# Kernel optimization log

Measured on AMD Instinct MI355X. Metric: run time of the kernel, lower is better.

The kernel has to match this reference:

```python
import math
import jax, jax.numpy as jnp
import numpy as np

DIM = 256; DEPTH = 5; FANOUT = 10; VOCAB = 257
B = 16; T = 2048
NEXP = 8; HID = 512; TOPK = 2; TEMP = 1.0; HEADS = 2
CAPACITY = math.ceil(B * TOPK / NEXP * 1.1)  # capacity-based dispatch, =5
LAYER_SIZES = [FANOUT ** l for l in range(DEPTH)]  # [1,10,100,1000,10000]


def setup_inputs() -> dict:
    key = jax.random.key(0)
    ks = iter(jax.random.split(key, 64))
    def p(shape, scale=0.02):
        return jax.random.normal(next(ks), shape, jnp.float32) * scale
    inp = {
        'tokens': jax.random.randint(next(ks), (B, T), 0, VOCAB),
        'embed': p((VOCAB, DIM)),
        'pin_w': p((DIM, DIM)), 'pin_b': jnp.zeros(DIM, jnp.float32),
        'pch_w': p((DIM, DIM)), 'pch_b': jnp.zeros(DIM, jnp.float32),
        'depth_bias': p((DEPTH, DIM)),
        'q_w': p((DIM, DIM)), 'q_b': jnp.zeros(DIM, jnp.float32),
        'k_w': p((DIM, DIM)), 'k_b': jnp.zeros(DIM, jnp.float32),
        'v_w': p((DIM, DIM)), 'v_b': jnp.zeros(DIM, jnp.float32),
        'o_w': p((DIM, DIM)), 'o_b': jnp.zeros(DIM, jnp.float32),
        'level_gate': jnp.zeros(DEPTH, jnp.float32),
        'depth_gate': jnp.zeros((DEPTH, DIM), jnp.float32),
        'in_proj_w': p((DIM, 3 * DIM)), 'in_proj_b': jnp.zeros(3 * DIM, jnp.float32),
        'out_proj_w': p((DIM, DIM)), 'out_proj_b': jnp.zeros(DIM, jnp.float32),
        'ln_g': jnp.ones(DIM, jnp.float32), 'ln_b': jnp.zeros(DIM, jnp.float32),
        'ic_gate': jnp.zeros(1, jnp.float32),
        'gate_w': p((DIM, NEXP)), 'gate_b': jnp.zeros(NEXP, jnp.float32),
        'ew1': p((NEXP, DIM, HID)), 'eb1': jnp.zeros((NEXP, HID), jnp.float32),
        'ew2': p((NEXP, HID, DIM)), 'eb2': jnp.zeros((NEXP, DIM), jnp.float32),
        'hw1': p((DIM, DIM)), 'hb1': jnp.zeros(DIM, jnp.float32),
        'hw2': p((DIM, VOCAB)), 'hb2': jnp.zeros(VOCAB, jnp.float32),
    }
    return inp


def _fractal(context, pin_w, pin_b, pch_w, pch_b, depth_bias, q_w, q_b, k_w, k_b,
             v_w, v_b, o_w, o_b, level_gate, depth_gate,
             in_proj_w, in_proj_b, out_proj_w, out_proj_b, ln_g, ln_b, ic_gate):
    Bc = context.shape[0]
    base = context @ pin_w + pin_b                       # [B,D]
    y_next = None
    level_means = [None] * DEPTH
    inv_sqrt_d = 1.0 / math.sqrt(DIM)
    for l in reversed(range(DEPTH)):
        n = LAYER_SIZES[l]
        if l == DEPTH - 1:
            child_agg = jnp.zeros((Bc, n, DIM), context.dtype)
        else:
            yg = y_next.reshape(Bc, n, FANOUT, DIM)      # children grouped per parent
            q = (base + depth_bias[l]) @ q_w + q_b       # [B,D], shared across nodes
            k = yg @ k_w + k_b
            v = yg @ v_w + v_b
            att = jax.nn.softmax(jnp.einsum('bd,bnfd->bnf', q, k) * inv_sqrt_d, axis=-1)
            child_agg = jax.nn.sigmoid(depth_gate[l]) * jnp.einsum('bnf,bnfd->bnd', att, v)
        gate = jax.nn.sigmoid(level_gate[l])
        upd = (base[:, None, :] + depth_bias[l][None, None, :] + child_agg @ pch_w + pch_b) * gate
        y = jax.nn.relu(upd) @ o_w + o_b                 # [B,n,D]
        level_means[l] = y.mean(axis=1)
        y_next = y
    root = y_next[:, 0, :]                               # n==1 at level 0
    # interconnect: MHA over per-level means [B,DEPTH,D]
    z = jnp.stack(level_means, axis=1)
    qkv = z @ in_proj_w + in_proj_b
    qh, kh, vh = jnp.split(qkv, 3, axis=-1)
    hd = DIM // HEADS
    def to_heads(t):
        return t.reshape(Bc, DEPTH, HEADS, hd).transpose(0, 2, 1, 3)
    qh, kh, vh = to_heads(qh), to_heads(kh), to_heads(vh)
    aw = jax.nn.softmax(jnp.einsum('bhqd,bhkd->bhqk', qh, kh) / math.sqrt(hd), axis=-1)
    z2 = jnp.einsum('bhqk,bhkd->bhqd', aw, vh).transpose(0, 2, 1, 3).reshape(Bc, DEPTH, DIM)
    z2 = z2 @ out_proj_w + out_proj_b
    zs = z + z2
    mu = zs.mean(-1, keepdims=True)
    var = ((zs - mu) ** 2).mean(-1, keepdims=True)
    zn = (zs - mu) / jnp.sqrt(var + 1e-5) * ln_g + ln_b
    return root + jax.nn.sigmoid(ic_gate) * zn[:, 0, :]


def _moe(ctx, gate_w, gate_b, ew1, eb1, ew2, eb2):
    scaled = (ctx @ gate_w + gate_b) / TEMP
    top_vals, top_idx = jax.lax.top_k(scaled, TOPK)      # [B,K]
    gs = jax.nn.softmax(top_vals, axis=-1)               # [B,K], strictly > 0
    out = jnp.zeros_like(ctx)
    for e in range(NEXP):                                # fixed small expert loop
        sflat = jnp.where(top_idx == e, gs, -1.0).reshape(-1)   # [B*K]
        vals, pos = jax.lax.top_k(sflat, CAPACITY)       # capacity-limited dispatch
        w = jnp.where(vals > 0.0, vals, 0.0)             # drop unassigned/overflow
        tok = pos // TOPK
        xin = ctx[tok]                                   # [cap,D]
        eo = jax.nn.relu(xin @ ew1[e] + eb1[e]) @ ew2[e] + eb2[e]
        out = out.at[tok].add(eo * w[:, None])
    return out


def reference(tokens, embed, pin_w, pin_b, pch_w, pch_b, depth_bias,
              q_w, q_b, k_w, k_b, v_w, v_b, o_w, o_b, level_gate, depth_gate,
              in_proj_w, in_proj_b, out_proj_w, out_proj_b, ln_g, ln_b, ic_gate,
              gate_w, gate_b, ew1, eb1, ew2, eb2, hw1, hb1, hw2, hb2):
    x = embed[tokens]                                    # [B,T,D]
    context = x.mean(axis=1)                             # [B,D]
    root = _fractal(context, pin_w, pin_b, pch_w, pch_b, depth_bias, q_w, q_b,
                    k_w, k_b, v_w, v_b, o_w, o_b, level_gate, depth_gate,
                    in_proj_w, in_proj_b, out_proj_w, out_proj_b, ln_g, ln_b, ic_gate)
    root = root + _moe(root, gate_w, gate_b, ew1, eb1, ew2, eb2)
    h = x + root[:, None, :]                             # per-token logits from context + token emb
    logits = jax.nn.relu(h @ hw1 + hb1) @ hw2 + hb2      # [B,T,V]
    return logits
```

## Files before the change

### kernel.cpp

```cpp
#include <hip/hip_runtime.h>
#include <hip/hip_bf16.h>
#include <math.h>

#define DIM    256
#define DEPTH  5
#define FANOUT 10
#define VOCAB  257
#define BB     16
#define TT     2048
#define NEXP   8
#define HID    512
#define TOPK   2
#define CAP    5

__device__ __forceinline__ float sigm(float x) { return 1.f / (1.f + expf(-x)); }

__device__ __forceinline__ void mv8x2(const float* sv, const float* __restrict__ W,
                                      int kseg, int cq, float red[16][DIM]) {
  const float* Wp = W + (size_t)kseg * 16 * DIM + cq * 4;
  float4 acc = {0.f, 0.f, 0.f, 0.f};
#pragma unroll 1
  for (int h = 0; h < 2; ++h) {
    float4 wv[8];
#pragma unroll
    for (int i = 0; i < 8; ++i)
      wv[i] = *(const float4*)(Wp + (size_t)(h * 8 + i) * DIM);
#pragma unroll
    for (int i = 0; i < 8; ++i) {
      float s = sv[kseg * 16 + h * 8 + i];
      acc.x = fmaf(s, wv[i].x, acc.x);
      acc.y = fmaf(s, wv[i].y, acc.y);
      acc.z = fmaf(s, wv[i].z, acc.z);
      acc.w = fmaf(s, wv[i].w, acc.w);
    }
    __builtin_amdgcn_sched_barrier(0);
  }
  *(float4*)&red[kseg][cq * 4] = acc;
}

__device__ __forceinline__ float sum16(const float red[16][DIM], int d) {
  float s = 0.f;
#pragma unroll
  for (int g = 0; g < 16; ++g) s += red[g][d];
  return s;
}

__global__ void __launch_bounds__(1024) k_fractal(
    const int* __restrict__ tokens, const float* __restrict__ embed,
    const float* __restrict__ pin_w, const float* __restrict__ pin_b,
    const float* __restrict__ pch_w, const float* __restrict__ pch_b,
    const float* __restrict__ depth_bias,
    const float* __restrict__ v_w, const float* __restrict__ v_b,
    const float* __restrict__ o_w, const float* __restrict__ o_b,
    const float* __restrict__ level_gate, const float* __restrict__ depth_gate,
    const float* __restrict__ in_proj_w, const float* __restrict__ in_proj_b,
    const float* __restrict__ out_proj_w, const float* __restrict__ out_proj_b,
    const float* __restrict__ ln_g, const float* __restrict__ ln_b,
    const float* __restrict__ ic_gate,
    float* __restrict__ rootA, float* __restrict__ root2,
    int* __restrict__ bidx, int* __restrict__ boff) {
  int bx = blockIdx.x;
  int tid = threadIdx.x;
  int xcd = bx & 7, slot = bx >> 3;
  __shared__ int cnt[VOCAB];
  __shared__ float sv[DIM];
  __shared__ float basev[DIM];
  __shared__ float ym[DEPTH][DIM];
  __shared__ float q0v[DIM], kh[DEPTH][DIM], vh[DEPTH][DIM];
  __shared__ float red11[4][11][DIM];
  __shared__ float zsv[DIM];
  __shared__ float aw[16];
  __shared__ float redl[8];
  __shared__ int offb[VOCAB + 1];
  __shared__ int woff[VOCAB];
  float (*red16)[DIM] = reinterpret_cast<float(*)[DIM]>(&red11[0][0][0]);

  if (xcd == 1) {
    if (slot < BB) {
      int b = slot;
      for (int i = tid; i < VOCAB; i += 1024) cnt[i] = 0;
      __syncthreads();
      for (int t = tid; t < TT; t += 1024) atomicAdd(&cnt[tokens[b * TT + t]], 1);
      __syncthreads();
      if (tid == 0) {
        int a = 0;
        for (int v = 0; v < VOCAB; ++v) { offb[v] = a; a += cnt[v]; }
        offb[VOCAB] = a;
      }
      __syncthreads();
      if (tid <= VOCAB) boff[b * (VOCAB + 1) + tid] = offb[tid];
      if (tid < VOCAB) woff[tid] = offb[tid];
      __syncthreads();
      for (int t = tid; t < TT; t += 1024) {
        int tok = tokens[b * TT + t];
        int p = atomicAdd(&woff[tok], 1);
        bidx[b * TT + p] = t;
      }
    }
    return;
  }
  if (xcd != 0) return;
  if (slot >= BB) {
    int w = slot - BB;
    float sx = 0.f, sy = 0.f, sz = 0.f, sw = 0.f;
#pragma unroll 1
    for (int q = 0; q < 3; ++q) {
      int r = w * 3 + q;
      if (r >= 37) break;
      const float* W; int n = 16384;
      if (r < 4)       W = pin_w      + (size_t)r * 16384;
      else if (r < 8)  W = pch_w      + (size_t)(r - 4) * 16384;
      else if (r < 12) W = v_w        + (size_t)(r - 8) * 16384;
      else if (r < 16) W = o_w        + (size_t)(r - 12) * 16384;
      else if (r < 20) W = out_proj_w + (size_t)(r - 16) * 16384;
      else if (r < 32) W = in_proj_w  + (size_t)(r - 20) * 16384;
      else { W = embed + (size_t)(r - 32) * 16384; n = 65792 - (r - 32) * 16384;
             if (n > 16384) n = 16384; }
      const float4* src = (const float4*)W + tid;
#pragma unroll
      for (int k = 0; k < 4; ++k) {
        int p = tid * 4 + k * 4096;
        if (p + 4 <= n) {
          float4 v = src[k * 1024];
          sx += v.x; sy += v.y; sz += v.z; sw += v.w;
        }
      }
    }
    asm volatile("" :: "v"(sx), "v"(sy), "v"(sz), "v"(sw));
    return;
  }

  int b = slot;
  int d = tid & 255;
  int ks = tid >> 8;
  int k0 = ks * 64;
  int kseg = tid >> 6;
  int cq = tid & 63;

  for (int i = tid; i < VOCAB; i += 1024) cnt[i] = 0;
  __syncthreads();
  for (int t = tid; t < TT; t += 1024) atomicAdd(&cnt[tokens[b * TT + t]], 1);
  __syncthreads();
  {
    const float* Ep = embed + (size_t)kseg * 16 * DIM + cq * 4;
    float4 acc = {0.f, 0.f, 0.f, 0.f};
#pragma unroll 1
    for (int h = 0; h < 2; ++h) {
      float4 ev[8];
#pragma unroll
      for (int i = 0; i < 8; ++i)
        ev[i] = *(const float4*)(Ep + (size_t)(h * 8 + i) * DIM);
#pragma unroll
      for (int i = 0; i < 8; ++i) {
        float cv = (float)cnt[kseg * 16 + h * 8 + i];
        acc.x = fmaf(cv, ev[i].x, acc.x);
        acc.y = fmaf(cv, ev[i].y, acc.y);
        acc.z = fmaf(cv, ev[i].z, acc.z);
        acc.w = fmaf(cv, ev[i].w, acc.w);
      }
      __builtin_amdgcn_sched_barrier(0);
    }
    *(float4*)&red16[kseg][cq * 4] = acc;
  }
  __syncthreads();
  if (ks == 0) {
    float s = sum16(red16, d);
    s = fmaf((float)cnt[256], embed[(size_t)256 * DIM + d], s);
    sv[d] = s * (1.0f / (float)TT);
  }
  __syncthreads();

  mv8x2(sv, pin_w, kseg, cq, red16);
  __syncthreads();
  if (ks == 0) {
    float base = sum16(red16, d) + pin_b[d];
    basev[d] = base;
    float u = (base + depth_bias[4 * DIM + d] + pch_b[d]) * sigm(level_gate[4]);
    sv[d] = fmaxf(u, 0.f);
  }
  __syncthreads();
  mv8x2(sv, o_w, kseg, cq, red16);
  __syncthreads();
  if (ks == 0) {
    float y = sum16(red16, d) + o_b[d];
    ym[4][d] = y;
    sv[d] = y;
  }
  __syncthreads();
  for (int l = 3; l >= 0; --l) {
    mv8x2(sv, v_w, kseg, cq, red16);
    __syncthreads();
    if (ks == 0) {
      float vv = sum16(red16, d) + v_b[d];
      sv[d] = sigm(depth_gate[l * DIM + d]) * vv;
    }
    __syncthreads();
    mv8x2(sv, pch_w, kseg, cq, red16);
    __syncthreads();
    if (ks == 0) {
      float t = sum16(red16, d) + pch_b[d];
      float u = (basev[d] + depth_bias[l * DIM + d] + t) * sigm(level_gate[l]);
      sv[d] = fmaxf(u, 0.f);
    }
    __syncthreads();
    mv8x2(sv, o_w, kseg, cq, red16);
    __syncthreads();
    if (ks == 0) {
      float y = sum16(red16, d) + o_b[d];
      ym[l][d] = y;
      sv[d] = y;
    }
    __syncthreads();
  }
  {
    float aq = 0.f;
    float ak0 = 0.f, ak1 = 0.f, ak2 = 0.f, ak3 = 0.f, ak4 = 0.f;
    float av0 = 0.f, av1 = 0.f, av2 = 0.f, av3 = 0.f, av4 = 0.f;
#pragma unroll
    for (int h = 0; h < 8; ++h) {
      int kb = k0 + h * 8;
      float wq[8], wk[8], wv8[8];
#pragma unroll
      for (int i = 0; i < 8; ++i) {
        const float* wrow = in_proj_w + (size_t)(kb + i) * 768;
        wq[i] = wrow[d]; wk[i] = wrow[256 + d]; wv8[i] = wrow[512 + d];
      }
#pragma unroll
      for (int i = 0; i < 8; ++i) {
        float z0 = ym[0][kb + i];
        aq  = fmaf(z0, wq[i], aq);
        ak0 = fmaf(z0, wk[i], ak0);
        av0 = fmaf(z0, wv8[i], av0);
        float z1 = ym[1][kb + i];
        ak1 = fmaf(z1, wk[i], ak1);
        av1 = fmaf(z1, wv8[i], av1);
        float z2 = ym[2][kb + i];
        ak2 = fmaf(z2, wk[i], ak2);
        av2 = fmaf(z2, wv8[i], av2);
        float z3 = ym[3][kb + i];
        ak3 = fmaf(z3, wk[i], ak3);
        av3 = fmaf(z3, wv8[i], av3);
        float z4 = ym[4][kb + i];
        ak4 = fmaf(z4, wk[i], ak4);
        av4 = fmaf(z4, wv8[i], av4);
      }
    }
    red11[ks][0][d] = ak0; red11[ks][1][d] = ak1; red11[ks][2][d] = ak2;
    red11[ks][3][d] = ak3; red11[ks][4][d] = ak4;
    red11[ks][5][d] = av0; red11[ks][6][d] = av1; red11[ks][7][d] = av2;
    red11[ks][8][d] = av3; red11[ks][9][d] = av4;
    red11[ks][10][d] = aq;
  }
  __syncthreads();
  for (int idx = tid; idx < 11 * DIM; idx += 1024) {
    int c = idx >> 8, dd = idx & 255;
    float sum = red11[0][c][dd] + red11[1][c][dd] + red11[2][c][dd] + red11[3][c][dd];
    if (c < 5)       kh[c][dd]     = sum + in_proj_b[256 + dd];
    else if (c < 10) vh[c - 5][dd] = sum + in_proj_b[512 + dd];
    else             q0v[dd]       = sum + in_proj_b[dd];
  }
  __syncthreads();
  {
    int wid = tid >> 6;
    if (wid < 10) {
      int h = wid / 5, l = wid - h * 5;
      int lane = tid & 63;
      float s = q0v[h * 128 + lane] * kh[l][h * 128 + lane];
      s = fmaf(q0v[h * 128 + 64 + lane], kh[l][h * 128 + 64 + lane], s);
      for (int o = 32; o > 0; o >>= 1) s += __shfl_down(s, o, 64);
      if (lane == 0) aw[wid] = s * 0.08838834764831845f;
    }
  }
  __syncthreads();
  if (tid < 2) {
    float m = aw[tid * 5];
    for (int l = 1; l < 5; ++l) m = fmaxf(m, aw[tid * 5 + l]);
    float e[5], ssum = 0.f;
    for (int l = 0; l < 5; ++l) { e[l] = expf(aw[tid * 5 + l] - m); ssum += e[l]; }
    for (int l = 0; l < 5; ++l) aw[tid * 5 + l] = e[l] / ssum;
  }
  __syncthreads();
  if (ks == 0) {
    int h = d >> 7;
    float z2 = 0.f;
    for (int l = 0; l < 5; ++l) z2 = fmaf(aw[h * 5 + l], vh[l][d], z2);
    sv[d] = z2;
  }
  __syncthreads();
  mv8x2(sv, out_proj_w, kseg, cq, red16);
  __syncthreads();
  if (ks == 0) {
    float z2p = sum16(red16, d) + out_proj_b[d];
    zsv[d] = ym[0][d] + z2p;
  }
  __syncthreads();
  float zs = 0.f, df = 0.f, mu = 0.f;
  if (tid < 256) {
    zs = zsv[tid];
    float v = zs;
    for (int o = 32; o > 0; o >>= 1) v += __shfl_down(v, o, 64);
    if ((tid & 63) == 0) redl[tid >> 6] = v;
  }
  __syncthreads();
  if (tid < 256) {
    mu = (redl[0] + redl[1] + redl[2] + redl[3]) * (1.f / 256.f);
    df = zs - mu;
  }
  __syncthreads();
  if (tid < 256) {
    float v = df * df;
    for (int o = 32; o > 0; o >>= 1) v += __shfl_down(v, o, 64);
    if ((tid & 63) == 0) redl[tid >> 6] = v;
  }
  __syncthreads();
  if (tid < 256) {
    float var = (redl[0] + redl[1] + redl[2] + redl[3]) * (1.f / 256.f);
    float zn = df / sqrtf(var + 1e-5f) * ln_g[tid] + ln_b[tid];
    float r = ym[0][tid] + sigm(ic_gate[0]) * zn;
    rootA[b * DIM + tid] = r;
    root2[b * DIM + tid] = r;
  }
}

__global__ void __launch_bounds__(256) k_moe(
    const float* __restrict__ rootA,
    const float* __restrict__ gate_w, const float* __restrict__ gate_b,
    const float* __restrict__ ew1, const float* __restrict__ eb1,
    const float* __restrict__ ew2, const float* __restrict__ eb2,
    float* __restrict__ root2) {
  int bx = blockIdx.x;
  int tid = threadIdx.x;
  if (bx >= 64) {
    int r = (bx - 64) % 128;
    const float* W = (r < 64) ? ew1 + (size_t)r * 16384
                              : ew2 + (size_t)(r - 64) * 16384;
    const float4* src = (const float4*)W + tid;
    float sx = 0.f, sy = 0.f, sz = 0.f, sw = 0.f;
#pragma unroll 4
    for (int i = 0; i < 16; ++i) {
      float4 v = src[i * 256];
      sx += v.x; sy += v.y; sz += v.z; sw += v.w;
    }
    asm volatile("" :: "v"(sx), "v"(sy), "v"(sz), "v"(sw));
    return;
  }
  int e = bx >> 3, jt = bx & 7, j0 = jt * 64;
  int w = tid >> 6, lane = tid & 63;
  __shared__ float rlds[BB * DIM];
  __shared__ float gwlds[DIM * NEXP];
  __shared__ float xin[CAP][DIM];
  __shared__ float red[CAP][4][64];
  __shared__ float hloc[CAP][64];
  __shared__ float sc[BB * NEXP];
  __shared__ float gs[BB * TOPK];
  __shared__ int gidx[BB * TOPK];
  __shared__ int stok[CAP];
  __shared__ float swt[CAP];
  for (int idx = tid; idx < BB * DIM / 4; idx += 256)
    *(float4*)&rlds[idx * 4] = *(const float4*)&rootA[idx * 4];
  for (int idx = tid; idx < DIM * NEXP / 4; idx += 256)
    *(float4*)&gwlds[idx * 4] = *(const float4*)&gate_w[idx * 4];
  __syncthreads();
  if (tid < BB * NEXP) {
    int b = tid >> 3, ep = tid & 7;
    float chunk[8];
#pragma unroll
    for (int g = 0; g < 8; ++g) {
      float acc = 0.f;
#pragma unroll 8
      for (int i = 0; i < 32; ++i) {
        int k = g * 32 + i;
        acc = fmaf(rlds[b * DIM + k], gwlds[k * NEXP + ep], acc);
      }
      chunk[g] = acc;
    }
    float s = gate_b[ep];
#pragma unroll
    for (int g = 0; g < 8; ++g) s += chunk[g];
    sc[tid] = s;
  }
  __syncthreads();
  if (tid < BB) {
    int bb = tid;
    int i0 = 0; float v0 = sc[bb * 8 + 0];
    for (int ee = 1; ee < 8; ++ee) { float v = sc[bb * 8 + ee]; if (v > v0) { v0 = v; i0 = ee; } }
    int i1 = -1; float v1 = -1e30f;
    for (int ee = 0; ee < 8; ++ee) {
      if (ee == i0) continue;
      float v = sc[bb * 8 + ee];
      if (v > v1) { v1 = v; i1 = ee; }
    }
    float e1v = expf(v1 - v0);
    float s = 1.f + e1v;
    gs[bb * 2 + 0] = 1.f / s;  gidx[bb * 2 + 0] = i0;
    gs[bb * 2 + 1] = e1v / s;  gidx[bb * 2 + 1] = i1;
  }
  __syncthreads();
  if (tid == 0) {
    unsigned used = 0u;
    for (int s = 0; s < CAP; ++s) {
      int bi = 0; float bv = -1e30f;
      for (int i = 0; i < 32; ++i) {
        if (used & (1u << i)) continue;
        float v = (gidx[i] == e) ? gs[i] : -1.0f;
        if (v > bv) { bv = v; bi = i; }
      }
      used |= (1u << bi);
      stok[s] = bi >> 1;
      swt[s] = bv > 0.f ? bv : 0.f;
    }
  }
  __syncthreads();
  for (int idx = tid; idx < CAP * DIM; idx += 256) {
    int s = idx >> 8, k = idx & 255;
    xin[s][k] = rlds[stok[s] * DIM + k];
  }
  __syncthreads();
  {
    float a0 = 0.f, a1 = 0.f, a2 = 0.f, a3 = 0.f, a4 = 0.f;
    const float* W = ew1 + (size_t)e * DIM * HID + j0 + lane;
    int kbase = w * 64;
#pragma unroll
    for (int h = 0; h < 8; ++h) {
      float wv[8];
#pragma unroll
      for (int i = 0; i < 8; ++i) wv[i] = W[(size_t)(kbase + h * 8 + i) * HID];
#pragma unroll
      for (int i = 0; i < 8; ++i) {
        int k = kbase + h * 8 + i;
        a0 = fmaf(xin[0][k], wv[i], a0);
        a1 = fmaf(xin[1][k], wv[i], a1);
        a2 = fmaf(xin[2][k], wv[i], a2);
        a3 = fmaf(xin[3][k], wv[i], a3);
        a4 = fmaf(xin[4][k], wv[i], a4);
      }
    }
    red[0][w][lane] = a0; red[1][w][lane] = a1; red[2][w][lane] = a2;
    red[3][w][lane] = a3; red[4][w][lane] = a4;
  }
  __syncthreads();
  for (int idx = tid; idx < CAP * 64; idx += 256) {
    int s = idx >> 6, j = idx & 63;
    float sum = red[s][0][j] + red[s][1][j] + red[s][2][j] + red[s][3][j]
              + eb1[e * HID + j0 + j];
    hloc[s][j] = fmaxf(sum, 0.f);
  }
  __syncthreads();
  {
    int d = tid;
    float a0 = 0.f, a1 = 0.f, a2 = 0.f, a3 = 0.f, a4 = 0.f;
    const float* W2 = ew2 + (size_t)e * HID * DIM + (size_t)j0 * DIM + d;
#pragma unroll
    for (int h = 0; h < 8; ++h) {
      float wv[8];
#pragma unroll
      for (int i = 0; i < 8; ++i) wv[i] = W2[(size_t)(h * 8 + i) * DIM];
#pragma unroll
      for (int i = 0; i < 8; ++i) {
        int j = h * 8 + i;
        a0 = fmaf(hloc[0][j], wv[i], a0);
        a1 = fmaf(hloc[1][j], wv[i], a1);
        a2 = fmaf(hloc[2][j], wv[i], a2);
        a3 = fmaf(hloc[3][j], wv[i], a3);
        a4 = fmaf(hloc[4][j], wv[i], a4);
      }
    }
    float bias = (jt == 0) ? eb2[e * DIM + d] : 0.f;
#pragma unroll
    for (int s = 0; s < CAP; ++s) {
      float as = (s == 0) ? a0 : (s == 1) ? a1 : (s == 2) ? a2 : (s == 3) ? a3 : a4;
      float wgt = swt[s];
      if (wgt > 0.f)
        atomicAdd(&root2[stok[s] * DIM + d], (as + bias) * wgt);
    }
  }
}

__global__ void __launch_bounds__(256) k_logits(
    const float* __restrict__ embed, const float* __restrict__ root2,
    const float* __restrict__ hw1, const float* __restrict__ hb1,
    const float* __restrict__ hw2, const float* __restrict__ hb2,
    const int* __restrict__ bidx, const int* __restrict__ boff,
    float* __restrict__ out) {
  int tok = blockIdx.x, r0 = blockIdx.y * 4;
  int c = threadIdx.x;
  __shared__ float hrow[4][DIM];
  __shared__ float hid[4][DIM];
  __shared__ float tailred[4][17];
  __shared__ float tailv[4];
  {
    float ev = embed[(size_t)tok * DIM + c];
#pragma unroll
    for (int j = 0; j < 4; ++j) hrow[j][c] = ev + root2[(size_t)(r0 + j) * DIM + c];
  }
  __syncthreads();
  {
    float a0 = hb1[c], a1 = a0, a2 = a0, a3 = a0;
    for (int kb = 0; kb < DIM; kb += 8) {
      float wv[8];
#pragma unroll
      for (int i = 0; i < 8; ++i) wv[i] = hw1[(size_t)(kb + i) * DIM + c];
#pragma unroll
      for (int i = 0; i < 8; ++i) {
        int k = kb + i;
        a0 = fmaf(hrow[0][k], wv[i], a0);
        a1 = fmaf(hrow[1][k], wv[i], a1);
        a2 = fmaf(hrow[2][k], wv[i], a2);
        a3 = fmaf(hrow[3][k], wv[i], a3);
      }
    }
    hid[0][c] = fmaxf(a0, 0.f); hid[1][c] = fmaxf(a1, 0.f);
    hid[2][c] = fmaxf(a2, 0.f); hid[3][c] = fmaxf(a3, 0.f);
  }
  __syncthreads();
  float a0, a1, a2, a3;
  {
    a0 = hb2[c]; a1 = a0; a2 = a0; a3 = a0;
    for (int kb = 0; kb < DIM; kb += 8) {
      float wv[8];
#pragma unroll
      for (int i = 0; i < 8; ++i) wv[i] = hw2[(size_t)(kb + i) * VOCAB + c];
#pragma unroll
      for (int i = 0; i < 8; ++i) {
        int k = kb + i;
        a0 = fmaf(hid[0][k], wv[i], a0);
        a1 = fmaf(hid[1][k], wv[i], a1);
        a2 = fmaf(hid[2][k], wv[i], a2);
        a3 = fmaf(hid[3][k], wv[i], a3);
      }
    }
  }
  if (c < 64) {
    int r = c >> 4, seg = c & 15;
    float sum = 0.f;
#pragma unroll 4
    for (int i = 0; i < 16; ++i) {
      int k = seg * 16 + i;
      sum = fmaf(hid[r][k], hw2[(size_t)k * VOCAB + 256], sum);
    }
    tailred[r][seg] = sum;
  }
  __syncthreads();
  if (c < 4) {
    float a = hb2[256];
#pragma unroll
    for (int s = 0; s < 16; ++s) a += tailred[c][s];
    tailv[c] = a;
  }
  __syncthreads();
#pragma unroll
  for (int j = 0; j < 4; ++j) {
    int b = r0 + j;
    int s = boff[b * (VOCAB + 1) + tok];
    int e = boff[b * (VOCAB + 1) + tok + 1];
    float aj = (j == 0) ? a0 : (j == 1) ? a1 : (j == 2) ? a2 : a3;
    float tl = tailv[j];
    for (int m = s; m < e; ++m) {
      int t = bidx[b * TT + m];
      size_t base = (size_t)(b * TT + t) * VOCAB;
      out[base + c] = aj;
      if (c == 0) out[base + 256] = tl;
    }
  }
}

extern "C" void kernel_launch(void* const* d_in, const int* in_sizes, int n_in,
                              void* d_out, int out_size, void* d_ws, size_t ws_size,
                              hipStream_t stream) {
  (void)in_sizes; (void)n_in; (void)out_size; (void)ws_size;
  const int*   tokens     = (const int*)d_in[0];
  const float* embed      = (const float*)d_in[1];
  const float* pin_w      = (const float*)d_in[2];
  const float* pin_b      = (const float*)d_in[3];
  const float* pch_w      = (const float*)d_in[4];
  const float* pch_b      = (const float*)d_in[5];
  const float* depth_bias = (const float*)d_in[6];
  const float* v_w        = (const float*)d_in[11];
  const float* v_b        = (const float*)d_in[12];
  const float* o_w        = (const float*)d_in[13];
  const float* o_b        = (const float*)d_in[14];
  const float* level_gate = (const float*)d_in[15];
  const float* depth_gate = (const float*)d_in[16];
  const float* in_proj_w  = (const float*)d_in[17];
  const float* in_proj_b  = (const float*)d_in[18];
  const float* out_proj_w = (const float*)d_in[19];
  const float* out_proj_b = (const float*)d_in[20];
  const float* ln_g       = (const float*)d_in[21];
  const float* ln_b       = (const float*)d_in[22];
  const float* ic_gate    = (const float*)d_in[23];
  const float* gate_w     = (const float*)d_in[24];
  const float* gate_b     = (const float*)d_in[25];
  const float* ew1        = (const float*)d_in[26];
  const float* eb1        = (const float*)d_in[27];
  const float* ew2        = (const float*)d_in[28];
  const float* eb2        = (const float*)d_in[29];
  const float* hw1        = (const float*)d_in[30];
  const float* hb1        = (const float*)d_in[31];
  const float* hw2        = (const float*)d_in[32];
  const float* hb2        = (const float*)d_in[33];
  float* out = (float*)d_out;

  float* ws      = (float*)d_ws;
  float* rootA   = ws + 4096;
  float* root2   = ws + 8192;
  int*   bidx    = (int*)(ws + 43136);
  int*   boff    = (int*)(ws + 75904);

  k_fractal<<<256, 1024, 0, stream>>>(tokens, embed, pin_w, pin_b, pch_w, pch_b,
                                      depth_bias, v_w, v_b, o_w, o_b, level_gate,
                                      depth_gate, in_proj_w, in_proj_b, out_proj_w,
                                      out_proj_b, ln_g, ln_b, ic_gate, rootA, root2,
                                      bidx, boff);
  k_moe<<<256, 256, 0, stream>>>(rootA, gate_w, gate_b, ew1, eb1,
                                 ew2, eb2, root2);
  k_logits<<<dim3(VOCAB, 4), 256, 0, stream>>>(embed, root2, hw1, hb1, hw2, hb2,
                                               bidx, boff, out);
}
```

Before: 230.6 us.

## Fold gated v_w and pch_w into per-level matrices built by helper blocks

Helper blocks inside the fractal kernel precompute, for each of the 4 inner levels, a combined matrix diag(sigmoid(depth_gate[l]))·v_w·pch_w plus a fused bias, and write them to workspace. The main per-batch blocks wait on a global flag and then do one matvec per level instead of two on the serial critical path. The remaining idle blocks on other XCDs are repurposed to prefetch expert and head weights into cache, and the MoE kernel's prefetch blocks now warm hw1/hw2/embed. The cost is extra matrix-matrix work, a spin-wait that relies on all producer blocks being co-resident, and a memset launch.

Result: slower. 494.5 us (+114.4%).

```diff
diff --git a/kernel.cpp b/kernel.cpp
--- a/kernel.cpp
+++ b/kernel.cpp
@@ -57,8 +57,12 @@
     const float* __restrict__ out_proj_w, const float* __restrict__ out_proj_b,
     const float* __restrict__ ln_g, const float* __restrict__ ln_b,
     const float* __restrict__ ic_gate,
+    const float* __restrict__ ew1, const float* __restrict__ ew2,
+    const float* __restrict__ hw1, const float* __restrict__ hw2,
     float* __restrict__ rootA, float* __restrict__ root2,
-    int* __restrict__ bidx, int* __restrict__ boff) {
+    int* __restrict__ bidx, int* __restrict__ boff,
+    float* __restrict__ wsW, float* __restrict__ wsb,
+    int* __restrict__ wflag) {
   int bx = blockIdx.x;
   int tid = threadIdx.x;
   int xcd = bx & 7, slot = bx >> 3;
@@ -73,8 +77,25 @@
   __shared__ float redl[8];
   __shared__ int offb[VOCAB + 1];
   __shared__ int woff[VOCAB];
+  __shared__ float vg[64][DIM];
+  __shared__ float gl[DIM];
   float (*red16)[DIM] = reinterpret_cast<float(*)[DIM]>(&red11[0][0][0]);
 
+  if (xcd >= 2) {
+    int wi = (xcd - 2) * 32 + slot;
+    int r = wi % 128;
+    const float* W = (r < 64) ? ew1 + (size_t)r * 16384
+                              : ew2 + (size_t)(r - 64) * 16384;
+    const float4* src = (const float4*)W + tid;
+    float sx = 0.f, sy = 0.f, sz = 0.f, sw = 0.f;
+#pragma unroll
+    for (int k2 = 0; k2 < 4; ++k2) {
+      float4 v = src[k2 * 1024];
+      sx += v.x; sy += v.y; sz += v.z; sw += v.w;
+    }
+    asm volatile("" :: "v"(sx), "v"(sy), "v"(sz), "v"(sw));
+    return;
+  }
   if (xcd == 1) {
     if (slot < BB) {
       int b = slot;
@@ -96,37 +117,88 @@
         int p = atomicAdd(&woff[tok], 1);
         bidx[b * TT + p] = t;
       }
+    } else {
+      int r = (slot - BB) % 12;
+      const float* W;
+      if (r < 4)       W = hw1   + (size_t)r * 16384;
+      else if (r < 8)  W = hw2   + (size_t)(r - 4) * 16384;
+      else             W = embed + (size_t)(r - 8) * 16384;
+      const float4* src = (const float4*)W + tid;
+      float sx = 0.f, sy = 0.f, sz = 0.f, sw = 0.f;
+#pragma unroll
+      for (int k2 = 0; k2 < 4; ++k2) {
+        float4 v = src[k2 * 1024];
+        sx += v.x; sy += v.y; sz += v.z; sw += v.w;
+      }
+      asm volatile("" :: "v"(sx), "v"(sy), "v"(sz), "v"(sw));
     }
     return;
   }
-  if (xcd != 0) return;
   if (slot >= BB) {
-    int w = slot - BB;
-    float sx = 0.f, sy = 0.f, sz = 0.f, sw = 0.f;
+    int p = slot - BB;
+    int l = p & 3, rowbase = (p >> 2) * 64;
+    int j = tid & 255, iq = tid >> 8;
+    if (tid < DIM) gl[tid] = sigm(depth_gate[l * DIM + tid]);
+    __syncthreads();
+    for (int idx = tid; idx < 64 * 64; idx += 1024) {
+      int i = idx >> 6, c4 = idx & 63;
+      float4 v = *(const float4*)&v_w[(size_t)(rowbase + i) * DIM + c4 * 4];
+      v.x *= gl[c4 * 4];     v.y *= gl[c4 * 4 + 1];
+      v.z *= gl[c4 * 4 + 2]; v.w *= gl[c4 * 4 + 3];
+      *(float4*)&vg[i][c4 * 4] = v;
+    }
+    if (tid < DIM) sv[tid] = v_b[tid] * gl[tid];
+    __syncthreads();
+    float acc[16];
+#pragma unroll
+    for (int r = 0; r < 16; ++r) acc[r] = 0.f;
+    float bacc = 0.f;
 #pragma unroll 1
-    for (int q = 0; q < 3; ++q) {
-      int r = w * 3 + q;
-      if (r >= 37) break;
-      const float* W; int n = 16384;
-      if (r < 4)       W = pin_w      + (size_t)r * 16384;
-      else if (r < 8)  W = pch_w      + (size_t)(r - 4) * 16384;
-      else if (r < 12) W = v_w        + (size_t)(r - 8) * 16384;
-      else if (r < 16) W = o_w        + (size_t)(r - 12) * 16384;
-      else if (r < 20) W = out_proj_w + (size_t)(r - 16) * 16384;
-      else if (r < 32) W = in_proj_w  + (size_t)(r - 20) * 16384;
-      else { W = embed + (size_t)(r - 32) * 16384; n = 65792 - (r - 32) * 16384;
-             if (n > 16384) n = 16384; }
-      const float4* src = (const float4*)W + tid;
-#pragma unroll
-      for (int k = 0; k < 4; ++k) {
-        int p = tid * 4 + k * 4096;
-        if (p + 4 <= n) {
-          float4 v = src[k * 1024];
+    for (int kb = 0; kb < DIM; kb += 16) {
+      float wv[16];
+#pragma unroll
+      for (int i = 0; i < 16; ++i) wv[i] = pch_w[(size_t)(kb + i) * DIM + j];
+#pragma unroll
+      for (int i = 0; i < 16; ++i) {
+        int k = kb + i;
+        float w = wv[i];
+#pragma unroll
+        for (int r = 0; r < 16; ++r)
+          acc[r] = fmaf(vg[iq * 16 + r][k], w, acc[r]);
+        bacc = fmaf(sv[k], w, bacc);
+      }
+      __builtin_amdgcn_sched_barrier(0);
+    }
+    float* Wl = wsW + (size_t)l * 65536;
+#pragma unroll
+    for (int r = 0; r < 16; ++r)
+      Wl[(size_t)(rowbase + iq * 16 + r) * DIM + j] = acc[r];
+    if (iq == 0 && (p >> 2) == 0)
+      wsb[l * DIM + j] = bacc + pch_b[j];
+    __threadfence();
+    __syncthreads();
+    if (tid == 0) atomicAdd(wflag, 1);
+    {
+      float sx = 0.f, sy = 0.f, sz = 0.f, sw = 0.f;
+#pragma unroll 1
+      for (int q = 0; q < 2; ++q) {
+        int r = p * 2 + q;
+        if (r >= 28) break;
+        const float* W;
+        if (r < 4)       W = o_w        + (size_t)r * 16384;
+        else if (r < 16) W = in_proj_w  + (size_t)(r - 4) * 16384;
+        else if (r < 20) W = out_proj_w + (size_t)(r - 16) * 16384;
+        else if (r < 24) W = pin_w      + (size_t)(r - 20) * 16384;
+        else             W = embed      + (size_t)(r - 24) * 16384;
+        const float4* src = (const float4*)W + tid;
+#pragma unroll
+        for (int k2 = 0; k2 < 4; ++k2) {
+          float4 v = src[k2 * 1024];
           sx += v.x; sy += v.y; sz += v.z; sw += v.w;
         }
       }
-    }
-    asm volatile("" :: "v"(sx), "v"(sy), "v"(sz), "v"(sw));
+      asm volatile("" :: "v"(sx), "v"(sy), "v"(sz), "v"(sw));
+    }
     return;
   }
 
@@ -187,18 +259,15 @@
     sv[d] = y;
   }
   __syncthreads();
+  if (tid == 0) {
+    while (__hip_atomic_load(wflag, __ATOMIC_ACQUIRE, __HIP_MEMORY_SCOPE_AGENT) < 16) {}
+  }
+  __syncthreads();
   for (int l = 3; l >= 0; --l) {
-    mv8x2(sv, v_w, kseg, cq, red16);
+    mv8x2(sv, wsW + (size_t)l * 65536, kseg, cq, red16);
     __syncthreads();
     if (ks == 0) {
-      float vv = sum16(red16, d) + v_b[d];
-      sv[d] = sigm(depth_gate[l * DIM + d]) * vv;
-    }
-    __syncthreads();
-    mv8x2(sv, pch_w, kseg, cq, red16);
-    __syncthreads();
-    if (ks == 0) {
-      float t = sum16(red16, d) + pch_b[d];
+      float t = sum16(red16, d) + wsb[l * DIM + d];
       float u = (basev[d] + depth_bias[l * DIM + d] + t) * sigm(level_gate[l]);
       sv[d] = fmaxf(u, 0.f);
     }
@@ -327,13 +396,17 @@
     const float* __restrict__ gate_w, const float* __restrict__ gate_b,
     const float* __restrict__ ew1, const float* __restrict__ eb1,
     const float* __restrict__ ew2, const float* __restrict__ eb2,
+    const float* __restrict__ hw1, const float* __restrict__ hw2,
+    const float* __restrict__ embed,
     float* __restrict__ root2) {
   int bx = blockIdx.x;
   int tid = threadIdx.x;
   if (bx >= 64) {
-    int r = (bx - 64) % 128;
-    const float* W = (r < 64) ? ew1 + (size_t)r * 16384
-                              : ew2 + (size_t)(r - 64) * 16384;
+    int r = (bx - 64) % 12;
+    const float* W;
+    if (r < 4)       W = hw1   + (size_t)r * 16384;
+    else if (r < 8)  W = hw2   + (size_t)(r - 4) * 16384;
+    else             W = embed + (size_t)(r - 8) * 16384;
     const float4* src = (const float4*)W + tid;
     float sx = 0.f, sy = 0.f, sz = 0.f, sw = 0.f;
 #pragma unroll 4
@@ -601,18 +674,23 @@
   float* out = (float*)d_out;
 
   float* ws      = (float*)d_ws;
+  int*   wflag   = (int*)ws;
   float* rootA   = ws + 4096;
   float* root2   = ws + 8192;
   int*   bidx    = (int*)(ws + 43136);
   int*   boff    = (int*)(ws + 75904);
-
+  float* wsW     = ws + 131072;
+  float* wsb     = ws + 393216;
+
+  hipMemsetAsync(wflag, 0, sizeof(int), stream);
   k_fractal<<<256, 1024, 0, stream>>>(tokens, embed, pin_w, pin_b, pch_w, pch_b,
                                       depth_bias, v_w, v_b, o_w, o_b, level_gate,
                                       depth_gate, in_proj_w, in_proj_b, out_proj_w,
-                                      out_proj_b, ln_g, ln_b, ic_gate, rootA, root2,
-                                      bidx, boff);
+                                      out_proj_b, ln_g, ln_b, ic_gate, ew1, ew2,
+                                      hw1, hw2, rootA, root2, bidx, boff,
+                                      wsW, wsb, wflag);
   k_moe<<<256, 256, 0, stream>>>(rootA, gate_w, gate_b, ew1, eb1,
-                                 ew2, eb2, root2);
+                                 ew2, eb2, hw1, hw2, embed, root2);
   k_logits<<<dim3(VOCAB, 4), 256, 0, stream>>>(embed, root2, hw1, hb1, hw2, hb2,
                                                bidx, boff, out);
 }
```
